# Optimization experiments

Hardware: AMD Instinct MI355X
Metric: run time of the kernel (lower is better)

## Reference

```python
import jax, jax.numpy as jnp
import numpy as np
from jax import lax

GAMMA = 1.0

def _conv(x, w, b, stride, pad):
    y = lax.conv_general_dilated(x, w, (stride, stride), [(pad, pad), (pad, pad)],
                                 dimension_numbers=('NCHW', 'OIHW', 'NCHW'))
    return y + b[None, :, None, None]

def _maxpool2s1(x):
    return lax.reduce_window(x, -jnp.inf, lax.max, (1, 1, 2, 2), (1, 1, 1, 1), 'VALID')

def setup_inputs() -> dict:
    key = jax.random.key(0)
    ks = jax.random.split(key, 13)
    d = {}
    d['x'] = jax.random.normal(ks[0], (128, 3, 250, 250), dtype=jnp.float32)
    d['conv1_w'] = jax.random.normal(ks[1], (6, 3, 5, 5), dtype=jnp.float32) / np.sqrt(3 * 25)
    d['conv1_b'] = jax.random.normal(ks[2], (6,), dtype=jnp.float32) * 0.01
    d['conv2_w'] = jax.random.normal(ks[3], (15, 6, 3, 3), dtype=jnp.float32) / np.sqrt(6 * 9)
    d['conv2_b'] = jax.random.normal(ks[4], (15,), dtype=jnp.float32) * 0.01
    d['fc1_w'] = jax.random.normal(ks[5], (120, 55815), dtype=jnp.float32) / np.sqrt(55815.0)
    d['fc1_b'] = jax.random.normal(ks[6], (120,), dtype=jnp.float32) * 0.01
    d['fc2_w'] = jax.random.normal(ks[7], (84, 120), dtype=jnp.float32) / np.sqrt(120.0)
    d['fc2_b'] = jax.random.normal(ks[8], (84,), dtype=jnp.float32) * 0.01
    d['fc3_w'] = jax.random.normal(ks[9], (1, 84), dtype=jnp.float32) / np.sqrt(84.0)
    d['fc3_b'] = jax.random.normal(ks[10], (1,), dtype=jnp.float32) * 0.01
    d['support'] = jax.random.normal(ks[11], (10, 1), dtype=jnp.float32)
    return d

def reference(x, conv1_w, conv1_b, conv2_w, conv2_b, fc1_w, fc1_b, fc2_w, fc2_b, fc3_w, fc3_b, support):
    h = jax.nn.relu(_conv(x, conv1_w, conv1_b, 2, 1))   # [B,6,124,124]
    h = _maxpool2s1(h)                                   # [B,6,123,123] (dropout = identity in eval)
    h = jax.nn.relu(_conv(h, conv2_w, conv2_b, 2, 1))    # [B,15,62,62]
    h = _maxpool2s1(h)                                   # [B,15,61,61]
    h = h.reshape(h.shape[0], -1)                        # [B,55815]
    h = jax.nn.relu(h @ fc1_w.T + fc1_b)
    h = jax.nn.relu(h @ fc2_w.T + fc2_b)
    h = h @ fc3_w.T + fc3_b                              # [B,1]
    # fused RBF kernel vs support set: k[i,j] = exp(-gamma*(x_i - s_j)^2)
    diff = h - support[:, 0][None, :]                    # [B,10]
    k = jnp.exp(-GAMMA * diff * diff)
    h = k.mean(axis=1, keepdims=True)                    # [B,1]
    probs = jax.nn.sigmoid(h)
    return jnp.concatenate((probs, 1.0 - probs), axis=-1)  # [B,2]
```

## Files before the change

kernel.cpp:

```cpp
#include <hip/hip_runtime.h>
#include <math.h>


#define BATCH 128

#define C1_ST 150
#define C1_TOT (37 * 133)
__global__ __launch_bounds__(256) void conv1_pool_kernel(
    const float* __restrict__ x, const float* __restrict__ w,
    const float* __restrict__ bias, float* __restrict__ out) {
  const int b = blockIdx.z;
  const int P0 = blockIdx.x * 64;
  const int R0 = blockIdx.y * 16;
  const int tid = threadIdx.x;
  const int t = tid >> 4;
  const int s = tid & 15;

  __shared__ float lds[37 * C1_ST];

  float acc0[5][6], acc1[5][6];
#pragma unroll
  for (int oc = 0; oc < 6; oc++) {
    float bv = bias[oc];
#pragma unroll
    for (int dc = 0; dc < 5; dc++) { acc0[dc][oc] = bv; acc1[dc][oc] = bv; }
  }

  const int ihb = 2 * R0 - 1, iwb = 2 * P0 - 1;

#pragma unroll 1
  for (int ci = 0; ci < 3; ci++) {
    __syncthreads();
    const float* src = x + (size_t)(b * 3 + ci) * 62500;
#pragma unroll 1
    for (int base = tid; base < C1_TOT; base += 2048) {
      float vv[8];
#pragma unroll
      for (int k = 0; k < 8; k++) {
        int i = base + (k << 8);
        int lr = i / 133, il = i - lr * 133;
        int ih = ihb + lr, iw = iwb + il;
        bool ok = (i < C1_TOT) && ((unsigned)ih < 250u) && ((unsigned)iw < 250u);
        vv[k] = ok ? src[ih * 250 + iw] : 0.f;
      }
#pragma unroll
      for (int k = 0; k < 8; k++) {
        int i = base + (k << 8);
        if (i < C1_TOT) {
          int lr = i / 133, il = i - lr * 133;
          lds[lr * C1_ST + il + (il >> 3)] = vv[k];
        }
      }
    }
    __syncthreads();

#pragma unroll 1
    for (int ir = 0; ir < 7; ir++) {
      const float* rp = &lds[(2 * t + ir) * C1_ST + 9 * s];
      float v[13];
#pragma unroll
      for (int j = 0; j < 13; j++) v[j] = rp[j + (j >> 3)];

      if (ir < 5) {
#pragma unroll
        for (int oc = 0; oc < 6; oc++) {
          const float* wr = w + ((oc * 3 + ci) * 5 + ir) * 5;
          float w0 = wr[0], w1 = wr[1], w2 = wr[2], w3 = wr[3], w4 = wr[4];
#pragma unroll
          for (int dc = 0; dc < 5; dc++) {
            float a = acc0[dc][oc];
            a += w0 * v[2 * dc + 0];
            a += w1 * v[2 * dc + 1];
            a += w2 * v[2 * dc + 2];
            a += w3 * v[2 * dc + 3];
            a += w4 * v[2 * dc + 4];
            acc0[dc][oc] = a;
          }
        }
      }
      if (ir >= 2) {
#pragma unroll
        for (int oc = 0; oc < 6; oc++) {
          const float* wr = w + ((oc * 3 + ci) * 5 + (ir - 2)) * 5;
          float w0 = wr[0], w1 = wr[1], w2 = wr[2], w3 = wr[3], w4 = wr[4];
#pragma unroll
          for (int dc = 0; dc < 5; dc++) {
            float a = acc1[dc][oc];
            a += w0 * v[2 * dc + 0];
            a += w1 * v[2 * dc + 1];
            a += w2 * v[2 * dc + 2];
            a += w3 * v[2 * dc + 3];
            a += w4 * v[2 * dc + 4];
            acc1[dc][oc] = a;
          }
        }
      }
    }
  }

  const int r = R0 + t;
  if (r < 123) {
#pragma unroll
    for (int oc = 0; oc < 6; oc++) {
      float* orow = out + ((size_t)(b * 6 + oc) * 123 + r) * 123;
#pragma unroll
      for (int i = 0; i < 4; i++) {
        int c = P0 + 4 * s + i;
        if (c < 123) {
          float m = fmaxf(fmaxf(acc0[i][oc], acc0[i + 1][oc]),
                          fmaxf(acc1[i][oc], acc1[i + 1][oc]));
          orow[c] = fmaxf(m, 0.f);
        }
      }
    }
  }
}

#define C2_ST 84
#define C2_TOT (35 * 67)
__global__ __launch_bounds__(256) void conv2_pool_kernel(
    const float* __restrict__ in, const float* __restrict__ w,
    const float* __restrict__ bias, float* __restrict__ out) {
  const int b = blockIdx.z;
  const int P0 = blockIdx.x * 32;
  const int R0 = blockIdx.y * 16;
  const int tid = threadIdx.x;
  const int t = tid >> 4;
  const int s = tid & 15;

  __shared__ float lds[35 * C2_ST];

  float acc0[3][15], acc1[3][15];
#pragma unroll
  for (int k = 0; k < 15; k++) {
    float bv = bias[k];
#pragma unroll
    for (int dc = 0; dc < 3; dc++) { acc0[dc][k] = bv; acc1[dc][k] = bv; }
  }

  const int ihb = 2 * R0 - 1, iwb = 2 * P0 - 1;

#pragma unroll 1
  for (int ci = 0; ci < 6; ci++) {
    __syncthreads();
    const float* src = in + (size_t)(b * 6 + ci) * 15129;
#pragma unroll 1
    for (int base = tid; base < C2_TOT; base += 2048) {
      float vv[8];
#pragma unroll
      for (int k = 0; k < 8; k++) {
        int i = base + (k << 8);
        int lr = i / 67, il = i - lr * 67;
        int ih = ihb + lr, iw = iwb + il;
        bool ok = (i < C2_TOT) && ((unsigned)ih < 123u) && ((unsigned)iw < 123u);
        vv[k] = ok ? src[ih * 123 + iw] : 0.f;
      }
#pragma unroll
      for (int k = 0; k < 8; k++) {
        int i = base + (k << 8);
        if (i < C2_TOT) {
          int lr = i / 67, il = i - lr * 67;
          lds[lr * C2_ST + il + (il >> 2)] = vv[k];
        }
      }
    }
    __syncthreads();

#pragma unroll 1
    for (int ir = 0; ir < 5; ir++) {
      const float* rp = &lds[(2 * t + ir) * C2_ST + 5 * s];
      float v[7];
#pragma unroll
      for (int j = 0; j < 7; j++) v[j] = rp[j + (j >> 2)];

      if (ir < 3) {
#pragma unroll
        for (int k = 0; k < 15; k++) {
          const float* wr = w + ((k * 6 + ci) * 3 + ir) * 3;
          float w0 = wr[0], w1 = wr[1], w2 = wr[2];
#pragma unroll
          for (int dc = 0; dc < 3; dc++) {
            float a = acc0[dc][k];
            a += w0 * v[2 * dc + 0];
            a += w1 * v[2 * dc + 1];
            a += w2 * v[2 * dc + 2];
            acc0[dc][k] = a;
          }
        }
      }
      if (ir >= 2) {
#pragma unroll
        for (int k = 0; k < 15; k++) {
          const float* wr = w + ((k * 6 + ci) * 3 + (ir - 2)) * 3;
          float w0 = wr[0], w1 = wr[1], w2 = wr[2];
#pragma unroll
          for (int dc = 0; dc < 3; dc++) {
            float a = acc1[dc][k];
            a += w0 * v[2 * dc + 0];
            a += w1 * v[2 * dc + 1];
            a += w2 * v[2 * dc + 2];
            acc1[dc][k] = a;
          }
        }
      }
    }
  }

  const int r = R0 + t;
  if (r < 61) {
#pragma unroll
    for (int k = 0; k < 15; k++) {
      float* orow = out + ((size_t)(b * 15 + k) * 61 + r) * 61;
#pragma unroll
      for (int i = 0; i < 2; i++) {
        int c = P0 + 2 * s + i;
        if (c < 61) {
          float m = fmaxf(fmaxf(acc0[i][k], acc0[i + 1][k]),
                          fmaxf(acc1[i][k], acc1[i + 1][k]));
          orow[c] = fmaxf(m, 0.f);
        }
      }
    }
  }
}

#define KTOT 55815
#define NPART 512
#define KCHUNK 112
__global__ __launch_bounds__(256) void fc1_splitk_kernel(
    const float* __restrict__ act, const float* __restrict__ w,
    float* __restrict__ partial) {
  const int kbase = blockIdx.x * KCHUNK;
  const int tid = threadIdx.x;
  const int tx = tid % 16, ty = tid / 16;
  __shared__ float ldsA[8 * 132];
  __shared__ float ldsB[8 * 132];
  float acc[8][8];
#pragma unroll
  for (int i = 0; i < 8; i++)
#pragma unroll
    for (int j = 0; j < 8; j++) acc[i][j] = 0.f;

  for (int s8 = 0; s8 < KCHUNK / 8; s8++) {
    int kofs = kbase + s8 * 8;
    __syncthreads();
    for (int i = tid; i < 1024; i += 256) {
      int m = i >> 3, kk = i & 7;
      int k = kofs + kk;
      ldsA[kk * 132 + m] = (k < KTOT) ? act[m * KTOT + k] : 0.f;
    }
    for (int i = tid; i < 960; i += 256) {
      int n = i >> 3, kk = i & 7;
      int k = kofs + kk;
      ldsB[kk * 132 + n] = (k < KTOT) ? w[n * KTOT + k] : 0.f;
    }
    __syncthreads();
#pragma unroll
    for (int kk = 0; kk < 8; kk++) {
      float4 a0 = *(const float4*)&ldsA[kk * 132 + ty * 8];
      float4 a1 = *(const float4*)&ldsA[kk * 132 + ty * 8 + 4];
      float4 b0 = *(const float4*)&ldsB[kk * 132 + tx * 8];
      float4 b1 = *(const float4*)&ldsB[kk * 132 + tx * 8 + 4];
      float av[8] = {a0.x, a0.y, a0.z, a0.w, a1.x, a1.y, a1.z, a1.w};
      float bv[8] = {b0.x, b0.y, b0.z, b0.w, b1.x, b1.y, b1.z, b1.w};
#pragma unroll
      for (int i = 0; i < 8; i++)
#pragma unroll
        for (int j = 0; j < 8; j++) acc[i][j] += av[i] * bv[j];
    }
  }

  float* dst = partial + (size_t)blockIdx.x * 15360;
#pragma unroll
  for (int i = 0; i < 8; i++) {
    int row = ty * 8 + i;
#pragma unroll
    for (int j = 0; j < 8; j++) {
      int col = tx * 8 + j;
      if (col < 120) dst[row * 120 + col] = acc[i][j];
    }
  }
}

__global__ __launch_bounds__(64) void fc1_reduce1_kernel(
    const float* __restrict__ partial, float* __restrict__ partial2) {
  int idx = blockIdx.x * 64 + threadIdx.x;
  int g = blockIdx.y;
  const float* p = partial + (size_t)g * 64 * 15360 + idx;
  float s = 0.f;
#pragma unroll 8
  for (int q = 0; q < 64; q++) s += p[(size_t)q * 15360];
  partial2[(size_t)g * 15360 + idx] = s;
}

__global__ __launch_bounds__(64) void fc1_reduce2_kernel(
    const float* __restrict__ partial2, const float* __restrict__ bias,
    float* __restrict__ h1) {
  int idx = blockIdx.x * 64 + threadIdx.x;
  float s = 0.f;
#pragma unroll
  for (int g = 0; g < 8; g++) s += partial2[(size_t)g * 15360 + idx];
  h1[idx] = fmaxf(s + bias[idx % 120], 0.f);
}

__global__ __launch_bounds__(128) void head_kernel(
    const float* __restrict__ h1, const float* __restrict__ fc2_w,
    const float* __restrict__ fc2_b, const float* __restrict__ fc3_w,
    const float* __restrict__ fc3_b, const float* __restrict__ support,
    float* __restrict__ out) {
  int b = blockIdx.x, t = threadIdx.x;
  __shared__ float hrow[120];
  __shared__ float s2[84];
  if (t < 120) hrow[t] = h1[b * 120 + t];
  __syncthreads();
  if (t < 84) {
    float d = fc2_b[t];
    for (int k = 0; k < 120; k++) d += fc2_w[t * 120 + k] * hrow[k];
    s2[t] = fmaxf(d, 0.f);
  }
  __syncthreads();
  if (t == 0) {
    float h = fc3_b[0];
    for (int j = 0; j < 84; j++) h += fc3_w[j] * s2[j];
    float ks = 0.f;
    for (int j = 0; j < 10; j++) {
      float diff = h - support[j];
      ks += expf(-diff * diff);
    }
    ks *= 0.1f;
    float p = 1.f / (1.f + expf(-ks));
    out[b * 2] = p;
    out[b * 2 + 1] = 1.f - p;
  }
}

extern "C" void kernel_launch(void* const* d_in, const int* in_sizes, int n_in,
                              void* d_out, int out_size, void* d_ws, size_t ws_size,
                              hipStream_t stream) {
  const float* x   = (const float*)d_in[0];
  const float* c1w = (const float*)d_in[1];
  const float* c1b = (const float*)d_in[2];
  const float* c2w = (const float*)d_in[3];
  const float* c2b = (const float*)d_in[4];
  const float* f1w = (const float*)d_in[5];
  const float* f1b = (const float*)d_in[6];
  const float* f2w = (const float*)d_in[7];
  const float* f2b = (const float*)d_in[8];
  const float* f3w = (const float*)d_in[9];
  const float* f3b = (const float*)d_in[10];
  const float* sup = (const float*)d_in[11];
  float* out = (float*)d_out;

  char* ws = (char*)d_ws;
  float* pool1 = (float*)ws;
  float* act   = (float*)(ws + 46476288);
  float* part  = (float*)ws;
  float* h1    = (float*)(ws + 33000000);
  float* part2 = (float*)(ws + 34000000);

  conv1_pool_kernel<<<dim3(2, 8, BATCH), 256, 0, stream>>>(x, c1w, c1b, pool1);
  conv2_pool_kernel<<<dim3(2, 4, BATCH), 256, 0, stream>>>(pool1, c2w, c2b, act);
  fc1_splitk_kernel<<<NPART, 256, 0, stream>>>(act, f1w, part);
  fc1_reduce1_kernel<<<dim3(240, 8), 64, 0, stream>>>(part, part2);
  fc1_reduce2_kernel<<<240, 64, 0, stream>>>(part2, f1b, h1);
  head_kernel<<<BATCH, 128, 0, stream>>>(h1, f2w, f2b, f3w, f3b, sup, out);
}
```

Before: 382.0 us.

## Split conv2 channels into groups, vectorize stores, widen fc1 blocks, use magic division

Conv2 now computes its output channels in two passes of 8 accumulators instead of 15. This cuts register pressure and should raise occupancy, but it loads the input tile twice, and channel 7 is computed redundantly in both passes. Both conv kernels replace integer division by 133 and 67 with multiply-shift and store pooled outputs as float4 or float2, even at unaligned row offsets. The fc1 split-K kernel moves to 512 threads with an 8x4 per-thread tile and float4 partial stores.

```diff
diff --git a/kernel.cpp b/kernel.cpp
--- a/kernel.cpp
+++ b/kernel.cpp
@@ -35,10 +35,13 @@
 #pragma unroll 1
     for (int base = tid; base < C1_TOT; base += 2048) {
       float vv[8];
+      int lrv[8], ilv[8];
 #pragma unroll
       for (int k = 0; k < 8; k++) {
         int i = base + (k << 8);
-        int lr = i / 133, il = i - lr * 133;
+        int lr = (int)(((unsigned)i * 63073u) >> 23);
+        int il = i - lr * 133;
+        lrv[k] = lr; ilv[k] = il;
         int ih = ihb + lr, iw = iwb + il;
         bool ok = (i < C1_TOT) && ((unsigned)ih < 250u) && ((unsigned)iw < 250u);
         vv[k] = ok ? src[ih * 250 + iw] : 0.f;
@@ -46,10 +49,7 @@
 #pragma unroll
       for (int k = 0; k < 8; k++) {
         int i = base + (k << 8);
-        if (i < C1_TOT) {
-          int lr = i / 133, il = i - lr * 133;
-          lds[lr * C1_ST + il + (il >> 3)] = vv[k];
-        }
+        if (i < C1_TOT) lds[lrv[k] * C1_ST + ilv[k] + (ilv[k] >> 3)] = vv[k];
       }
     }
     __syncthreads();
@@ -99,18 +99,26 @@
   }
 
   const int r = R0 + t;
+  const int c0 = P0 + 4 * s;
   if (r < 123) {
 #pragma unroll
     for (int oc = 0; oc < 6; oc++) {
       float* orow = out + ((size_t)(b * 6 + oc) * 123 + r) * 123;
-#pragma unroll
-      for (int i = 0; i < 4; i++) {
-        int c = P0 + 4 * s + i;
-        if (c < 123) {
-          float m = fmaxf(fmaxf(acc0[i][oc], acc0[i + 1][oc]),
-                          fmaxf(acc1[i][oc], acc1[i + 1][oc]));
-          orow[c] = fmaxf(m, 0.f);
-        }
+      float m0 = fmaxf(fmaxf(fmaxf(acc0[0][oc], acc0[1][oc]),
+                             fmaxf(acc1[0][oc], acc1[1][oc])), 0.f);
+      float m1 = fmaxf(fmaxf(fmaxf(acc0[1][oc], acc0[2][oc]),
+                             fmaxf(acc1[1][oc], acc1[2][oc])), 0.f);
+      float m2 = fmaxf(fmaxf(fmaxf(acc0[2][oc], acc0[3][oc]),
+                             fmaxf(acc1[2][oc], acc1[3][oc])), 0.f);
+      float m3 = fmaxf(fmaxf(fmaxf(acc0[3][oc], acc0[4][oc]),
+                             fmaxf(acc1[3][oc], acc1[4][oc])), 0.f);
+      if (c0 + 3 < 123) {
+        float4 st = make_float4(m0, m1, m2, m3);
+        *(float4*)&orow[c0] = st;
+      } else {
+        if (c0 < 123) orow[c0] = m0;
+        if (c0 + 1 < 123) orow[c0 + 1] = m1;
+        if (c0 + 2 < 123) orow[c0 + 2] = m2;
       }
     }
   }
@@ -130,94 +138,101 @@
 
   __shared__ float lds[35 * C2_ST];
 
-  float acc0[3][15], acc1[3][15];
-#pragma unroll
-  for (int k = 0; k < 15; k++) {
-    float bv = bias[k];
-#pragma unroll
-    for (int dc = 0; dc < 3; dc++) { acc0[dc][k] = bv; acc1[dc][k] = bv; }
-  }
-
   const int ihb = 2 * R0 - 1, iwb = 2 * P0 - 1;
-
-#pragma unroll 1
-  for (int ci = 0; ci < 6; ci++) {
-    __syncthreads();
-    const float* src = in + (size_t)(b * 6 + ci) * 15129;
-#pragma unroll 1
-    for (int base = tid; base < C2_TOT; base += 2048) {
-      float vv[8];
+  const int r = R0 + t;
+  const int c0 = P0 + 2 * s;
+
+#pragma unroll 1
+  for (int ocg = 0; ocg < 2; ocg++) {
+    const int oc0 = ocg * 7;
+    float acc0[3][8], acc1[3][8];
+#pragma unroll
+    for (int k = 0; k < 8; k++) {
+      float bv = bias[oc0 + k];
+#pragma unroll
+      for (int dc = 0; dc < 3; dc++) { acc0[dc][k] = bv; acc1[dc][k] = bv; }
+    }
+
+#pragma unroll 1
+    for (int ci = 0; ci < 6; ci++) {
+      __syncthreads();
+      const float* src = in + (size_t)(b * 6 + ci) * 15129;
+#pragma unroll 1
+      for (int base = tid; base < C2_TOT; base += 2048) {
+        float vv[8];
+        int lrv[8], ilv[8];
+#pragma unroll
+        for (int k = 0; k < 8; k++) {
+          int i = base + (k << 8);
+          int lr = (int)(((unsigned)i * 125204u) >> 23);
+          int il = i - lr * 67;
+          lrv[k] = lr; ilv[k] = il;
+          int ih = ihb + lr, iw = iwb + il;
+          bool ok = (i < C2_TOT) && ((unsigned)ih < 123u) && ((unsigned)iw < 123u);
+          vv[k] = ok ? src[ih * 123 + iw] : 0.f;
+        }
+#pragma unroll
+        for (int k = 0; k < 8; k++) {
+          int i = base + (k << 8);
+          if (i < C2_TOT) lds[lrv[k] * C2_ST + ilv[k] + (ilv[k] >> 2)] = vv[k];
+        }
+      }
+      __syncthreads();
+
+#pragma unroll 1
+      for (int ir = 0; ir < 5; ir++) {
+        const float* rp = &lds[(2 * t + ir) * C2_ST + 5 * s];
+        float v[7];
+#pragma unroll
+        for (int j = 0; j < 7; j++) v[j] = rp[j + (j >> 2)];
+
+        if (ir < 3) {
+#pragma unroll
+          for (int k = 0; k < 8; k++) {
+            const float* wr = w + (((oc0 + k) * 6 + ci) * 3 + ir) * 3;
+            float w0 = wr[0], w1 = wr[1], w2 = wr[2];
+#pragma unroll
+            for (int dc = 0; dc < 3; dc++) {
+              float a = acc0[dc][k];
+              a += w0 * v[2 * dc + 0];
+              a += w1 * v[2 * dc + 1];
+              a += w2 * v[2 * dc + 2];
+              acc0[dc][k] = a;
+            }
+          }
+        }
+        if (ir >= 2) {
+#pragma unroll
+          for (int k = 0; k < 8; k++) {
+            const float* wr = w + (((oc0 + k) * 6 + ci) * 3 + (ir - 2)) * 3;
+            float w0 = wr[0], w1 = wr[1], w2 = wr[2];
+#pragma unroll
+            for (int dc = 0; dc < 3; dc++) {
+              float a = acc1[dc][k];
+              a += w0 * v[2 * dc + 0];
+              a += w1 * v[2 * dc + 1];
+              a += w2 * v[2 * dc + 2];
+              acc1[dc][k] = a;
+            }
+          }
+        }
+      }
+    }
+
+    if (r < 61) {
 #pragma unroll
       for (int k = 0; k < 8; k++) {
-        int i = base + (k << 8);
-        int lr = i / 67, il = i - lr * 67;
-        int ih = ihb + lr, iw = iwb + il;
-        bool ok = (i < C2_TOT) && ((unsigned)ih < 123u) && ((unsigned)iw < 123u);
-        vv[k] = ok ? src[ih * 123 + iw] : 0.f;
-      }
-#pragma unroll
-      for (int k = 0; k < 8; k++) {
-        int i = base + (k << 8);
-        if (i < C2_TOT) {
-          int lr = i / 67, il = i - lr * 67;
-          lds[lr * C2_ST + il + (il >> 2)] = vv[k];
-        }
-      }
-    }
-    __syncthreads();
-
-#pragma unroll 1
-    for (int ir = 0; ir < 5; ir++) {
-      const float* rp = &lds[(2 * t + ir) * C2_ST + 5 * s];
-      float v[7];
-#pragma unroll
-      for (int j = 0; j < 7; j++) v[j] = rp[j + (j >> 2)];
-
-      if (ir < 3) {
-#pragma unroll
-        for (int k = 0; k < 15; k++) {
-          const float* wr = w + ((k * 6 + ci) * 3 + ir) * 3;
-          float w0 = wr[0], w1 = wr[1], w2 = wr[2];
-#pragma unroll
-          for (int dc = 0; dc < 3; dc++) {
-            float a = acc0[dc][k];
-            a += w0 * v[2 * dc + 0];
-            a += w1 * v[2 * dc + 1];
-            a += w2 * v[2 * dc + 2];
-            acc0[dc][k] = a;
-          }
-        }
-      }
-      if (ir >= 2) {
-#pragma unroll
-        for (int k = 0; k < 15; k++) {
-          const float* wr = w + ((k * 6 + ci) * 3 + (ir - 2)) * 3;
-          float w0 = wr[0], w1 = wr[1], w2 = wr[2];
-#pragma unroll
-          for (int dc = 0; dc < 3; dc++) {
-            float a = acc1[dc][k];
-            a += w0 * v[2 * dc + 0];
-            a += w1 * v[2 * dc + 1];
-            a += w2 * v[2 * dc + 2];
-            acc1[dc][k] = a;
-          }
-        }
-      }
-    }
-  }
-
-  const int r = R0 + t;
-  if (r < 61) {
-#pragma unroll
-    for (int k = 0; k < 15; k++) {
-      float* orow = out + ((size_t)(b * 15 + k) * 61 + r) * 61;
-#pragma unroll
-      for (int i = 0; i < 2; i++) {
-        int c = P0 + 2 * s + i;
-        if (c < 61) {
-          float m = fmaxf(fmaxf(acc0[i][k], acc0[i + 1][k]),
-                          fmaxf(acc1[i][k], acc1[i + 1][k]));
-          orow[c] = fmaxf(m, 0.f);
+        int oc = oc0 + k;
+        float* orow = out + ((size_t)(b * 15 + oc) * 61 + r) * 61;
+        float m0 = fmaxf(fmaxf(fmaxf(acc0[0][k], acc0[1][k]),
+                               fmaxf(acc1[0][k], acc1[1][k])), 0.f);
+        float m1 = fmaxf(fmaxf(fmaxf(acc0[1][k], acc0[2][k]),
+                               fmaxf(acc1[1][k], acc1[2][k])), 0.f);
+        if (c0 + 1 < 61) {
+          float2 st = make_float2(m0, m1);
+          *(float2*)&orow[c0] = st;
+        } else if (c0 < 61) {
+          orow[c0] = m0;
         }
       }
     }
@@ -227,29 +242,29 @@
 #define KTOT 55815
 #define NPART 512
 #define KCHUNK 112
-__global__ __launch_bounds__(256) void fc1_splitk_kernel(
+__global__ __launch_bounds__(512) void fc1_splitk_kernel(
     const float* __restrict__ act, const float* __restrict__ w,
     float* __restrict__ partial) {
   const int kbase = blockIdx.x * KCHUNK;
   const int tid = threadIdx.x;
-  const int tx = tid % 16, ty = tid / 16;
+  const int tx = tid & 31, ty = tid >> 5;
   __shared__ float ldsA[8 * 132];
   __shared__ float ldsB[8 * 132];
-  float acc[8][8];
+  float acc[8][4];
 #pragma unroll
   for (int i = 0; i < 8; i++)
 #pragma unroll
-    for (int j = 0; j < 8; j++) acc[i][j] = 0.f;
+    for (int j = 0; j < 4; j++) acc[i][j] = 0.f;
 
   for (int s8 = 0; s8 < KCHUNK / 8; s8++) {
     int kofs = kbase + s8 * 8;
     __syncthreads();
-    for (int i = tid; i < 1024; i += 256) {
+    for (int i = tid; i < 1024; i += 512) {
       int m = i >> 3, kk = i & 7;
       int k = kofs + kk;
       ldsA[kk * 132 + m] = (k < KTOT) ? act[m * KTOT + k] : 0.f;
     }
-    for (int i = tid; i < 960; i += 256) {
+    for (int i = tid; i < 960; i += 512) {
       int n = i >> 3, kk = i & 7;
       int k = kofs + kk;
       ldsB[kk * 132 + n] = (k < KTOT) ? w[n * KTOT + k] : 0.f;
@@ -259,25 +274,23 @@
     for (int kk = 0; kk < 8; kk++) {
       float4 a0 = *(const float4*)&ldsA[kk * 132 + ty * 8];
       float4 a1 = *(const float4*)&ldsA[kk * 132 + ty * 8 + 4];
-      float4 b0 = *(const float4*)&ldsB[kk * 132 + tx * 8];
-      float4 b1 = *(const float4*)&ldsB[kk * 132 + tx * 8 + 4];
+      float4 b0 = *(const float4*)&ldsB[kk * 132 + tx * 4];
       float av[8] = {a0.x, a0.y, a0.z, a0.w, a1.x, a1.y, a1.z, a1.w};
-      float bv[8] = {b0.x, b0.y, b0.z, b0.w, b1.x, b1.y, b1.z, b1.w};
+      float bv[4] = {b0.x, b0.y, b0.z, b0.w};
 #pragma unroll
       for (int i = 0; i < 8; i++)
 #pragma unroll
-        for (int j = 0; j < 8; j++) acc[i][j] += av[i] * bv[j];
-    }
-  }
-
-  float* dst = partial + (size_t)blockIdx.x * 15360;
-#pragma unroll
-  for (int i = 0; i < 8; i++) {
-    int row = ty * 8 + i;
-#pragma unroll
-    for (int j = 0; j < 8; j++) {
-      int col = tx * 8 + j;
-      if (col < 120) dst[row * 120 + col] = acc[i][j];
+        for (int j = 0; j < 4; j++) acc[i][j] += av[i] * bv[j];
+    }
+  }
+
+  if (tx < 30) {
+    float* dst = partial + (size_t)blockIdx.x * 15360;
+#pragma unroll
+    for (int i = 0; i < 8; i++) {
+      int row = ty * 8 + i;
+      float4 st = make_float4(acc[i][0], acc[i][1], acc[i][2], acc[i][3]);
+      *(float4*)&dst[row * 120 + tx * 4] = st;
     }
   }
 }
@@ -360,7 +373,7 @@
 
   conv1_pool_kernel<<<dim3(2, 8, BATCH), 256, 0, stream>>>(x, c1w, c1b, pool1);
   conv2_pool_kernel<<<dim3(2, 4, BATCH), 256, 0, stream>>>(pool1, c2w, c2b, act);
-  fc1_splitk_kernel<<<NPART, 256, 0, stream>>>(act, f1w, part);
+  fc1_splitk_kernel<<<NPART, 512, 0, stream>>>(act, f1w, part);
   fc1_reduce1_kernel<<<dim3(240, 8), 64, 0, stream>>>(part, part2);
   fc1_reduce2_kernel<<<240, 64, 0, stream>>>(part2, f1b, h1);
   head_kernel<<<BATCH, 128, 0, stream>>>(h1, f2w, f2b, f3w, f3b, sup, out);
```

New measurement: 360.7 us. 5.6% less time.
